# Kernel optimization log

Measured on AMD Instinct MI355X. Metric: run time of the kernel, lower is better.

## Reference

```python
import jax, jax.numpy as jnp
import numpy as np

N_RAYS, N_SAMPLES, GRID, APP_DIM, FEATC = 2048, 256, 128, 27, 128
VIEWPE, FEAPE = 2, 2
NEAR, FAR = 2.0, 6.0
AABB0, AABB1 = -1.5, 1.5
DENSITY_SHIFT, DISTANCE_SCALE = -10.0, 25.0
IN_MLPC = 2 * VIEWPE * 3 + 2 * FEAPE * APP_DIM + 3 + APP_DIM  # 150


def positional_encoding(x, freqs):
    fb = (2.0 ** jnp.arange(freqs)).astype(x.dtype)
    p = (x[..., None] * fb).reshape(x.shape[:-1] + (freqs * x.shape[-1],))
    return jnp.concatenate([jnp.sin(p), jnp.cos(p)], axis=-1)


def trilinear(vol, coords):
    # vol: [C, D, H, W]; coords: [P, 3] in [-1, 1] ordered (x, y, z) like torch grid_sample (align_corners=True)
    C, D, H, W = vol.shape
    x = (coords[:, 0] + 1.0) * 0.5 * (W - 1)
    y = (coords[:, 1] + 1.0) * 0.5 * (H - 1)
    z = (coords[:, 2] + 1.0) * 0.5 * (D - 1)
    x0 = jnp.clip(jnp.floor(x), 0, W - 2).astype(jnp.int32)
    y0 = jnp.clip(jnp.floor(y), 0, H - 2).astype(jnp.int32)
    z0 = jnp.clip(jnp.floor(z), 0, D - 2).astype(jnp.int32)
    x1, y1, z1 = x0 + 1, y0 + 1, z0 + 1
    fx, fy, fz = x - x0, y - y0, z - z0
    g = lambda zi, yi, xi: vol[:, zi, yi, xi]  # [C, P]
    out = (g(z0, y0, x0) * ((1 - fz) * (1 - fy) * (1 - fx))
           + g(z0, y0, x1) * ((1 - fz) * (1 - fy) * fx)
           + g(z0, y1, x0) * ((1 - fz) * fy * (1 - fx))
           + g(z0, y1, x1) * ((1 - fz) * fy * fx)
           + g(z1, y0, x0) * (fz * (1 - fy) * (1 - fx))
           + g(z1, y0, x1) * (fz * (1 - fy) * fx)
           + g(z1, y1, x0) * (fz * fy * (1 - fx))
           + g(z1, y1, x1) * (fz * fy * fx))
    return out  # [C, P]


def setup_inputs() -> dict:
    key = jax.random.key(0)
    ks = jax.random.split(key, 10)
    return {
        'rays_o': jax.random.uniform(ks[0], (N_RAYS, 3), jnp.float32, -0.5, 0.5) + jnp.array([0.0, 0.0, -4.0]),
        'rays_d': jax.random.normal(ks[1], (N_RAYS, 3), jnp.float32) * 0.1 + jnp.array([0.0, 0.0, 1.0]),
        'density_volume': jax.random.normal(ks[2], (1, GRID, GRID, GRID), jnp.float32) * 2.0 + 10.0,
        'app_volume': jax.random.normal(ks[3], (APP_DIM, GRID, GRID, GRID), jnp.float32) * 0.1,
        'w1': jax.random.normal(ks[4], (IN_MLPC, FEATC), jnp.float32) * 0.05,
        'b1': jnp.zeros((FEATC,), jnp.float32),
        'w2': jax.random.normal(ks[5], (FEATC, FEATC), jnp.float32) * 0.05,
        'b2': jnp.zeros((FEATC,), jnp.float32),
        'w3': jax.random.normal(ks[6], (FEATC, 3), jnp.float32) * 0.05,
        'b3': jnp.zeros((3,), jnp.float32),
    }


def reference(rays_o, rays_d, density_volume, app_volume, w1, b1, w2, b2, w3, b3):
    viewdirs = rays_d / jnp.linalg.norm(rays_d, axis=-1, keepdims=True)  # [N, 3]
    z_vals = jnp.linspace(NEAR, FAR, N_SAMPLES, dtype=rays_o.dtype)      # [S]
    z_vals = jnp.broadcast_to(z_vals, (N_RAYS, N_SAMPLES))
    pts = rays_o[:, None, :] + viewdirs[:, None, :] * z_vals[..., None]  # [N, S, 3]
    dists = jnp.concatenate([z_vals[:, 1:] - z_vals[:, :-1], z_vals[:, -1:] * 0 + (FAR - NEAR) / (N_SAMPLES - 1)], axis=-1)

    # normalize_coord: (xyz - aabb0) * (2 / aabbSize) - 1
    coords = jnp.clip((pts - AABB0) * (2.0 / (AABB1 - AABB0)) - 1.0, -1.0, 1.0).reshape(-1, 3)

    # density lookup + feature2density (softplus with shift)
    sigma_feat = trilinear(density_volume, coords)[0].reshape(N_RAYS, N_SAMPLES)
    sigma = jax.nn.softplus(sigma_feat + DENSITY_SHIFT)

    # raw2alpha: alpha, cumprod transmittance, weights
    alpha = 1.0 - jnp.exp(-sigma * dists * DISTANCE_SCALE)               # [N, S]
    T = jnp.cumprod(jnp.concatenate([jnp.ones((N_RAYS, 1), alpha.dtype), 1.0 - alpha + 1e-10], axis=-1), axis=-1)
    weights = alpha * T[:, :-1]                                          # [N, S]

    # MLPRender_Fea shading on all sampled points
    feat = trilinear(app_volume, coords).T                               # [P, app_dim]
    vd = jnp.broadcast_to(viewdirs[:, None, :], (N_RAYS, N_SAMPLES, 3)).reshape(-1, 3)
    mlp_in = jnp.concatenate([feat, vd, positional_encoding(feat, FEAPE), positional_encoding(vd, VIEWPE)], axis=-1)
    h = jax.nn.relu(mlp_in @ w1 + b1)
    h = jax.nn.relu(h @ w2 + b2)
    rgb = jax.nn.sigmoid(h @ w3 + b3).reshape(N_RAYS, N_SAMPLES, 3)

    acc_map = jnp.sum(weights, axis=-1)                                  # [N]
    rgb_map = jnp.sum(weights[..., None] * rgb, axis=-2)                 # [N, 3]
    rgb_map = jnp.clip(rgb_map + (1.0 - acc_map)[..., None], 0.0, 1.0)   # white background
    return rgb_map
```

## Files before the change

kernel.cpp:

```cpp
#include <hip/hip_runtime.h>
#include <math.h>

#define N_RAYS 2048
#define NSAMP  256
#define NPTS   (N_RAYS * NSAMP)
#define NCHUNK (NPTS / 64)
#define GRIDN  128
#define G2     (GRIDN * GRIDN)
#define G3     (GRIDN * GRIDN * GRIDN)
#define APPC   27
#define CHP    28
#define FEATC  128
#define K1PAD  160
#define ASTR   168
#define HSTR   136
#define H2STR  132

typedef __attribute__((ext_vector_type(8))) short short8;
typedef __attribute__((ext_vector_type(4))) float float4v;

__device__ __forceinline__ unsigned short f2bf(float f) {
  unsigned int u = __float_as_uint(f);
  return (unsigned short)((u + 0x7FFFu + ((u >> 16) & 1u)) >> 16);
}
__device__ __forceinline__ float bf2f(unsigned short u) {
  return __uint_as_float(((unsigned int)u) << 16);
}

__device__ __forceinline__ void corner_setup(float cx, float cy, float cz,
                                             int& ibase, float* w8) {
  float x = (cx + 1.0f) * 0.5f * 127.0f;
  float y = (cy + 1.0f) * 0.5f * 127.0f;
  float z = (cz + 1.0f) * 0.5f * 127.0f;
  float x0f = fminf(fmaxf(floorf(x), 0.0f), 126.0f);
  float y0f = fminf(fmaxf(floorf(y), 0.0f), 126.0f);
  float z0f = fminf(fmaxf(floorf(z), 0.0f), 126.0f);
  int x0 = (int)x0f, y0 = (int)y0f, z0 = (int)z0f;
  float fx = x - x0f, fy = y - y0f, fz = z - z0f;
  float gx = 1.0f - fx, gy = 1.0f - fy, gz = 1.0f - fz;
  ibase = (z0 * GRIDN + y0) * GRIDN + x0;
  w8[0] = gz * gy * gx; w8[1] = gz * gy * fx;
  w8[2] = gz * fy * gx; w8[3] = gz * fy * fx;
  w8[4] = fz * gy * gx; w8[5] = fz * gy * fx;
  w8[6] = fz * fy * gx; w8[7] = fz * fy * fx;
}

__global__ __launch_bounds__(256)
void transpose_kernel(const float* __restrict__ avol, unsigned short* __restrict__ appT) {
  int v0 = (blockIdx.x * 256 + threadIdx.x) * 2;
  float2 v[APPC];
  #pragma unroll
  for (int c = 0; c < APPC; ++c) v[c] = *(const float2*)&avol[(size_t)c * G3 + v0];
  unsigned short* dst = appT + (size_t)v0 * CHP;
  #pragma unroll
  for (int i = 0; i < 7; ++i) {
    ushort4 o;
    o.x = f2bf(v[4*i+0].x); o.y = f2bf(v[4*i+1].x);
    o.z = (4*i+2 < APPC) ? f2bf(v[4*i+2].x) : (unsigned short)0;
    o.w = (4*i+3 < APPC) ? f2bf(v[4*i+3].x) : (unsigned short)0;
    *(ushort4*)&dst[4*i] = o;
  }
  #pragma unroll
  for (int i = 0; i < 7; ++i) {
    ushort4 o;
    o.x = f2bf(v[4*i+0].y); o.y = f2bf(v[4*i+1].y);
    o.z = (4*i+2 < APPC) ? f2bf(v[4*i+2].y) : (unsigned short)0;
    o.w = (4*i+3 < APPC) ? f2bf(v[4*i+3].y) : (unsigned short)0;
    *(ushort4*)&dst[CHP + 4*i] = o;
  }
}

__global__ __launch_bounds__(256)
void prep_weights(const float* __restrict__ w1, const float* __restrict__ w2,
                  unsigned short* __restrict__ w1T, unsigned short* __restrict__ w2T) {
  int t = blockIdx.x * 256 + threadIdx.x;
  if (t < 128 * K1PAD) {
    int n = t / K1PAD, k = t - n * K1PAD;
    w1T[t] = (k < 150) ? f2bf(w1[k * 128 + n]) : (unsigned short)0;
  } else {
    int i = t - 128 * K1PAD;
    if (i < 128 * 128) {
      int n = i >> 7, k = i & 127;
      w2T[i] = f2bf(w2[k * 128 + n]);
    }
  }
}

__global__ __launch_bounds__(256)
void ray_kernel(const float* __restrict__ rays_o, const float* __restrict__ rays_d,
                const float* __restrict__ dvol,
                float* __restrict__ weights_ws, float* __restrict__ acc_ws,
                int* __restrict__ count, int* __restrict__ worklist) {
  int r = blockIdx.x, s = threadIdx.x;
  int lane = s & 63, wv = s >> 6;
  float ox = rays_o[r*3+0], oy = rays_o[r*3+1], oz = rays_o[r*3+2];
  float dx = rays_d[r*3+0], dy = rays_d[r*3+1], dz = rays_d[r*3+2];
  float inv = rsqrtf(dx*dx + dy*dy + dz*dz);
  dx *= inv; dy *= inv; dz *= inv;
  float z = 2.0f + (4.0f / 255.0f) * (float)s;
  float px = ox + dx * z, py = oy + dy * z, pz = oz + dz * z;
  float cx = fminf(fmaxf((px + 1.5f) * (2.0f/3.0f) - 1.0f, -1.0f), 1.0f);
  float cy = fminf(fmaxf((py + 1.5f) * (2.0f/3.0f) - 1.0f, -1.0f), 1.0f);
  float cz = fminf(fmaxf((pz + 1.5f) * (2.0f/3.0f) - 1.0f, -1.0f), 1.0f);
  int ibase; float w8[8];
  corner_setup(cx, cy, cz, ibase, w8);
  float sf = dvol[ibase]            * w8[0] + dvol[ibase + 1]            * w8[1]
           + dvol[ibase + GRIDN]    * w8[2] + dvol[ibase + GRIDN + 1]    * w8[3]
           + dvol[ibase + G2]       * w8[4] + dvol[ibase + G2 + 1]       * w8[5]
           + dvol[ibase + G2+GRIDN] * w8[6] + dvol[ibase + G2+GRIDN+1]   * w8[7];
  float xv = sf - 10.0f;
  float sp = (xv > 0.0f) ? (xv + log1pf(expf(-xv))) : log1pf(expf(xv));
  float alpha = 1.0f - expf(-sp * (100.0f / 255.0f));

  float tt = 1.0f - alpha + 1e-10f;
  float p = tt;
  #pragma unroll
  for (int d = 1; d < 64; d <<= 1) {
    float v = __shfl_up(p, d);
    if (lane >= d) p *= v;
  }
  __shared__ float wtot[4], wacc[4];
  if (lane == 63) wtot[wv] = p;
  __syncthreads();
  float pref = 1.0f;
  #pragma unroll
  for (int w2i = 0; w2i < 3; ++w2i) if (w2i < wv) pref *= wtot[w2i];
  float ex = __shfl_up(p, 1);
  if (lane == 0) ex = 1.0f;
  float T = pref * ex;
  float wgt = alpha * T;
  weights_ws[r * NSAMP + s] = wgt;
  float sum = wgt;
  #pragma unroll
  for (int d = 32; d; d >>= 1) sum += __shfl_xor(sum, d);
  if (lane == 0) {
    wacc[wv] = sum;
    if (sum >= 1e-5f) {
      int pos = atomicAdd(count, 1);
      worklist[pos] = r * 4 + wv;
    }
  }
  __syncthreads();
  if (s == 0) acc_ws[r] = wacc[0] + wacc[1] + wacc[2] + wacc[3];
}

template <bool USET>
__global__ __launch_bounds__(256)
void shade_kernel(const float* __restrict__ rays_o, const float* __restrict__ rays_d,
                  const float* __restrict__ avol, const unsigned short* __restrict__ appT,
                  const unsigned short* __restrict__ w1T, const unsigned short* __restrict__ w2T,
                  const float* __restrict__ b1, const float* __restrict__ b2,
                  const float* __restrict__ w3, const float* __restrict__ b3,
                  const float* __restrict__ weights_ws, float* __restrict__ rgb_accum,
                  const int* __restrict__ count, int* __restrict__ work_ctr,
                  const int* __restrict__ worklist) {
  __shared__ unsigned short A_lds[64 * ASTR];
  __shared__ unsigned short h1_lds[64 * HSTR];
  __shared__ int s_idx, s_n;

  int t = threadIdx.x;
  int lane = t & 63, wv = t >> 6;

  if (t == 0) s_n = *count;

  for (;;) {
    __syncthreads();
    if (t == 0) s_idx = atomicAdd(work_ctr, 1);
    __syncthreads();
    if (s_idx >= s_n) break;
    int chunk = worklist[s_idx];
    int gp0 = chunk * 64;
    int r = gp0 >> 8;

    {
      int q = t & 3, pt = t >> 2;
      int gp = gp0 + pt, s = gp & 255;
      float ox = rays_o[r*3+0], oy = rays_o[r*3+1], oz = rays_o[r*3+2];
      float dx = rays_d[r*3+0], dy = rays_d[r*3+1], dz = rays_d[r*3+2];
      float inv = rsqrtf(dx*dx + dy*dy + dz*dz);
      dx *= inv; dy *= inv; dz *= inv;
      float z = 2.0f + (4.0f / 255.0f) * (float)s;
      float px = ox + dx * z, py = oy + dy * z, pz = oz + dz * z;
      float cx = fminf(fmaxf((px + 1.5f) * (2.0f/3.0f) - 1.0f, -1.0f), 1.0f);
      float cy = fminf(fmaxf((py + 1.5f) * (2.0f/3.0f) - 1.0f, -1.0f), 1.0f);
      float cz = fminf(fmaxf((pz + 1.5f) * (2.0f/3.0f) - 1.0f, -1.0f), 1.0f);
      int ibase; float w8[8];
      corner_setup(cx, cy, cz, ibase, w8);

      int vi = ibase + (q >> 1) * G2 + (q & 1) * GRIDN;
      float wA = w8[2*q], wB = w8[2*q+1];
      float part[27];
      if (USET) {
        const ushort4* c0 = (const ushort4*)(appT + (size_t)vi * CHP);
        const ushort4* c1 = (const ushort4*)(appT + (size_t)(vi + 1) * CHP);
        ushort4 a[7], b[7];
        #pragma unroll
        for (int i = 0; i < 7; ++i) { a[i] = c0[i]; b[i] = c1[i]; }
        #pragma unroll
        for (int c = 0; c < 27; ++c) {
          unsigned short ua = (&a[c >> 2].x)[c & 3];
          unsigned short ub = (&b[c >> 2].x)[c & 3];
          part[c] = wA * bf2f(ua) + wB * bf2f(ub);
        }
      } else {
        #pragma unroll
        for (int c = 0; c < 27; ++c) {
          const float* base = avol + (size_t)c * G3 + vi;
          part[c] = wA * base[0] + wB * base[1];
        }
      }
      #pragma unroll
      for (int c = 0; c < 27; ++c) {
        float v = part[c];
        v += __shfl_xor(v, 1);
        v += __shfl_xor(v, 2);
        part[c] = v;
      }
      float f[7];
      #pragma unroll
      for (int j = 0; j < 7; ++j) {
        float vlo = (q & 1) ? part[7 + j] : part[j];
        float vhi = (q & 1) ? part[(21 + j < 27) ? 21 + j : 26] : part[14 + j];
        f[j] = (q & 2) ? vhi : vlo;
      }
      unsigned short* Arow = A_lds + pt * ASTR;
      int cbase = 7 * q;
      #pragma unroll
      for (int j = 0; j < 7; ++j) {
        int c = cbase + j;
        if (c < 27) {
          float fv = f[j];
          Arow[c] = f2bf(fv);
          float s1 = __sinf(fv),      c1 = __cosf(fv);
          float s2 = __sinf(2.0f*fv), c2 = __cosf(2.0f*fv);
          Arow[30 + 2*c] = f2bf(s1); Arow[31 + 2*c] = f2bf(s2);
          Arow[84 + 2*c] = f2bf(c1); Arow[85 + 2*c] = f2bf(c2);
        }
      }
      if (q == 3) {
        float vd[3] = {dx, dy, dz};
        #pragma unroll
        for (int d = 0; d < 3; ++d) {
          Arow[27 + d] = f2bf(vd[d]);
          float s1 = __sinf(vd[d]),      c1 = __cosf(vd[d]);
          float s2 = __sinf(2.0f*vd[d]), c2 = __cosf(2.0f*vd[d]);
          Arow[138 + 2*d] = f2bf(s1); Arow[139 + 2*d] = f2bf(s2);
          Arow[144 + 2*d] = f2bf(c1); Arow[145 + 2*d] = f2bf(c2);
        }
      }
      if (q == 1) {
        #pragma unroll
        for (int i = 0; i < 5; ++i) *(unsigned int*)&Arow[150 + 2*i] = 0u;
      }
    }
    __syncthreads();

    int nlo = lane & 15;
    int koff = (lane >> 4) * 8;
    int mrow = wv * 16 + nlo;

    short8 a1[5];
    #pragma unroll
    for (int kt = 0; kt < 5; ++kt)
      a1[kt] = *(const short8*)&A_lds[mrow * ASTR + kt * 32 + koff];
    #pragma unroll
    for (int nt = 0; nt < 8; ++nt) {
      float4v acc = {0.f, 0.f, 0.f, 0.f};
      #pragma unroll
      for (int kt = 0; kt < 5; ++kt) {
        short8 b = *(const short8*)&w1T[(nt * 16 + nlo) * K1PAD + kt * 32 + koff];
        acc = __builtin_amdgcn_mfma_f32_16x16x32_bf16(a1[kt], b, acc, 0, 0, 0);
      }
      float bv = b1[nt * 16 + nlo];
      #pragma unroll
      for (int rg = 0; rg < 4; ++rg) {
        int m = wv * 16 + (lane >> 4) * 4 + rg;
        float hv = fmaxf(acc[rg] + bv, 0.0f);
        h1_lds[m * HSTR + nt * 16 + nlo] = f2bf(hv);
      }
    }
    __syncthreads();

    short8 a2[4];
    #pragma unroll
    for (int kt = 0; kt < 4; ++kt)
      a2[kt] = *(const short8*)&h1_lds[mrow * HSTR + kt * 32 + koff];
    unsigned short* h2 = A_lds;
    #pragma unroll
    for (int nt = 0; nt < 8; ++nt) {
      float4v acc = {0.f, 0.f, 0.f, 0.f};
      #pragma unroll
      for (int kt = 0; kt < 4; ++kt) {
        short8 b = *(const short8*)&w2T[(nt * 16 + nlo) * FEATC + kt * 32 + koff];
        acc = __builtin_amdgcn_mfma_f32_16x16x32_bf16(a2[kt], b, acc, 0, 0, 0);
      }
      float bv = b2[nt * 16 + nlo];
      #pragma unroll
      for (int rg = 0; rg < 4; ++rg) {
        int m = wv * 16 + (lane >> 4) * 4 + rg;
        float hv = fmaxf(acc[rg] + bv, 0.0f);
        h2[m * H2STR + nt * 16 + nlo] = f2bf(hv);
      }
    }
    __syncthreads();

    if (wv < 3) {
      int j = wv, pp = lane;
      const unsigned short* h2row = h2 + pp * H2STR;
      float sum = b3[j];
      #pragma unroll
      for (int k = 0; k < FEATC; k += 4) {
        ushort4 hv = *(const ushort4*)&h2row[k];
        sum += bf2f(hv.x) * w3[(k+0)*3 + j] + bf2f(hv.y) * w3[(k+1)*3 + j]
             + bf2f(hv.z) * w3[(k+2)*3 + j] + bf2f(hv.w) * w3[(k+3)*3 + j];
      }
      float val = (1.0f / (1.0f + __expf(-sum))) * weights_ws[gp0 + pp];
      #pragma unroll
      for (int d = 32; d; d >>= 1) val += __shfl_xor(val, d);
      if (pp == 0) atomicAdd(&rgb_accum[r * 3 + j], val);
    }
  }
}

__global__ void finish_kernel(const float* __restrict__ rgb_accum,
                              const float* __restrict__ acc_ws,
                              float* __restrict__ out) {
  int i = blockIdx.x * blockDim.x + threadIdx.x;
  if (i < N_RAYS * 3) {
    int r = i / 3;
    float v = rgb_accum[i] + 1.0f - acc_ws[r];
    out[i] = fminf(fmaxf(v, 0.0f), 1.0f);
  }
}

extern "C" void kernel_launch(void* const* d_in, const int* in_sizes, int n_in,
                              void* d_out, int out_size, void* d_ws, size_t ws_size,
                              hipStream_t stream) {
  const float* rays_o = (const float*)d_in[0];
  const float* rays_d = (const float*)d_in[1];
  const float* dvol   = (const float*)d_in[2];
  const float* avol   = (const float*)d_in[3];
  const float* w1     = (const float*)d_in[4];
  const float* b1     = (const float*)d_in[5];
  const float* w2     = (const float*)d_in[6];
  const float* b2     = (const float*)d_in[7];
  const float* w3     = (const float*)d_in[8];
  const float* b3     = (const float*)d_in[9];
  float* out = (float*)d_out;

  float* weights_ws = (float*)d_ws;
  float* acc_ws     = weights_ws + NPTS;
  float* rgb_accum  = acc_ws + N_RAYS;
  int*   count      = (int*)(rgb_accum + N_RAYS * 3);
  int*   work_ctr   = count + 1;
  int*   worklist   = work_ctr + 1;
  unsigned short* w1T = (unsigned short*)(worklist + NCHUNK);
  unsigned short* w2T = w1T + 128 * K1PAD;
  unsigned short* appT = w2T + 128 * 128;

  size_t fixed_bytes = (size_t)(NPTS + N_RAYS + N_RAYS * 3 + 2 + NCHUNK) * 4
                     + (size_t)(128 * K1PAD + 128 * 128) * 2;
  size_t need = fixed_bytes + (size_t)G3 * CHP * 2;
  bool uset = ws_size >= need;

  hipMemsetAsync(rgb_accum, 0, (N_RAYS * 3 + 2) * sizeof(float), stream);
  prep_weights<<<(128 * K1PAD + 128 * 128 + 255) / 256, 256, 0, stream>>>(w1, w2, w1T, w2T);
  if (uset)
    transpose_kernel<<<G3 / 512, 256, 0, stream>>>(avol, appT);
  ray_kernel<<<N_RAYS, 256, 0, stream>>>(rays_o, rays_d, dvol, weights_ws, acc_ws,
                                         count, worklist);
  if (uset)
    shade_kernel<true><<<1024, 256, 0, stream>>>(rays_o, rays_d, avol, appT, w1T, w2T,
                                                 b1, b2, w3, b3, weights_ws, rgb_accum,
                                                 count, work_ctr, worklist);
  else
    shade_kernel<false><<<1024, 256, 0, stream>>>(rays_o, rays_d, avol, appT, w1T, w2T,
                                                  b1, b2, w3, b3, weights_ws, rgb_accum,
                                                  count, work_ctr, worklist);
  finish_kernel<<<(N_RAYS * 3 + 255) / 256, 256, 0, stream>>>(rgb_accum, acc_ws, out);
}
```

Before: 513.4 us.

## Restrict app-volume transpose to bounding box of active sample voxels

The ray kernel now also reduces per-wave min/max voxel indices for active chunks and atomically writes a global bounding box. The transpose that converts the appearance volume to bf16 channel-last layout runs after the ray kernel and skips voxels outside that box, cutting the read of the full 27-channel float volume. It also changes the H2STR LDS stride. The cost is extra shuffles and atomics in the ray kernel and a serial dependency: the transpose can no longer overlap with the ray pass.

```diff
diff --git a/kernel.cpp b/kernel.cpp
--- a/kernel.cpp
+++ b/kernel.cpp
@@ -14,7 +14,7 @@
 #define K1PAD  160
 #define ASTR   168
 #define HSTR   136
-#define H2STR  132
+#define H2STR  130
 
 typedef __attribute__((ext_vector_type(8))) short short8;
 typedef __attribute__((ext_vector_type(4))) float float4v;
@@ -27,15 +27,16 @@
   return __uint_as_float(((unsigned int)u) << 16);
 }
 
-__device__ __forceinline__ void corner_setup(float cx, float cy, float cz,
-                                             int& ibase, float* w8) {
+__device__ __forceinline__ void corner_setup_xyz(float cx, float cy, float cz,
+                                                 int& x0, int& y0, int& z0,
+                                                 int& ibase, float* w8) {
   float x = (cx + 1.0f) * 0.5f * 127.0f;
   float y = (cy + 1.0f) * 0.5f * 127.0f;
   float z = (cz + 1.0f) * 0.5f * 127.0f;
   float x0f = fminf(fmaxf(floorf(x), 0.0f), 126.0f);
   float y0f = fminf(fmaxf(floorf(y), 0.0f), 126.0f);
   float z0f = fminf(fmaxf(floorf(z), 0.0f), 126.0f);
-  int x0 = (int)x0f, y0 = (int)y0f, z0 = (int)z0f;
+  x0 = (int)x0f; y0 = (int)y0f; z0 = (int)z0f;
   float fx = x - x0f, fy = y - y0f, fz = z - z0f;
   float gx = 1.0f - fx, gy = 1.0f - fy, gz = 1.0f - fz;
   ibase = (z0 * GRIDN + y0) * GRIDN + x0;
@@ -46,8 +47,91 @@
 }
 
 __global__ __launch_bounds__(256)
-void transpose_kernel(const float* __restrict__ avol, unsigned short* __restrict__ appT) {
-  int v0 = (blockIdx.x * 256 + threadIdx.x) * 2;
+void ray_kernel(const float* __restrict__ rays_o, const float* __restrict__ rays_d,
+                const float* __restrict__ dvol,
+                float* __restrict__ weights_ws, float* __restrict__ acc_ws,
+                int* __restrict__ count, int* __restrict__ worklist,
+                int* __restrict__ bounds) {
+  int r = blockIdx.x, s = threadIdx.x;
+  int lane = s & 63, wv = s >> 6;
+  float ox = rays_o[r*3+0], oy = rays_o[r*3+1], oz = rays_o[r*3+2];
+  float dx = rays_d[r*3+0], dy = rays_d[r*3+1], dz = rays_d[r*3+2];
+  float inv = rsqrtf(dx*dx + dy*dy + dz*dz);
+  dx *= inv; dy *= inv; dz *= inv;
+  float z = 2.0f + (4.0f / 255.0f) * (float)s;
+  float px = ox + dx * z, py = oy + dy * z, pz = oz + dz * z;
+  float cx = fminf(fmaxf((px + 1.5f) * (2.0f/3.0f) - 1.0f, -1.0f), 1.0f);
+  float cy = fminf(fmaxf((py + 1.5f) * (2.0f/3.0f) - 1.0f, -1.0f), 1.0f);
+  float cz = fminf(fmaxf((pz + 1.5f) * (2.0f/3.0f) - 1.0f, -1.0f), 1.0f);
+  int x0, y0, z0, ibase; float w8[8];
+  corner_setup_xyz(cx, cy, cz, x0, y0, z0, ibase, w8);
+  float sf = dvol[ibase]            * w8[0] + dvol[ibase + 1]            * w8[1]
+           + dvol[ibase + GRIDN]    * w8[2] + dvol[ibase + GRIDN + 1]    * w8[3]
+           + dvol[ibase + G2]       * w8[4] + dvol[ibase + G2 + 1]       * w8[5]
+           + dvol[ibase + G2+GRIDN] * w8[6] + dvol[ibase + G2+GRIDN+1]   * w8[7];
+  float xv = sf - 10.0f;
+  float sp = (xv > 0.0f) ? (xv + log1pf(expf(-xv))) : log1pf(expf(xv));
+  float alpha = 1.0f - expf(-sp * (100.0f / 255.0f));
+
+  float tt = 1.0f - alpha + 1e-10f;
+  float p = tt;
+  #pragma unroll
+  for (int d = 1; d < 64; d <<= 1) {
+    float v = __shfl_up(p, d);
+    if (lane >= d) p *= v;
+  }
+  __shared__ float wtot[4], wacc[4];
+  if (lane == 63) wtot[wv] = p;
+  __syncthreads();
+  float pref = 1.0f;
+  #pragma unroll
+  for (int w2i = 0; w2i < 3; ++w2i) if (w2i < wv) pref *= wtot[w2i];
+  float ex = __shfl_up(p, 1);
+  if (lane == 0) ex = 1.0f;
+  float T = pref * ex;
+  float wgt = alpha * T;
+  weights_ws[r * NSAMP + s] = wgt;
+
+  float sum = wgt;
+  int mnx = x0, mny = y0, mnz = z0, mxx = x0, mxy = y0, mxz = z0;
+  #pragma unroll
+  for (int d = 32; d; d >>= 1) {
+    sum += __shfl_xor(sum, d);
+    mnx = min(mnx, __shfl_xor(mnx, d)); mxx = max(mxx, __shfl_xor(mxx, d));
+    mny = min(mny, __shfl_xor(mny, d)); mxy = max(mxy, __shfl_xor(mxy, d));
+    mnz = min(mnz, __shfl_xor(mnz, d)); mxz = max(mxz, __shfl_xor(mxz, d));
+  }
+  if (lane == 0) {
+    wacc[wv] = sum;
+    if (sum >= 1e-5f) {
+      int pos = atomicAdd(count, 1);
+      worklist[pos] = r * 4 + wv;
+      atomicMin(&bounds[0], mnx); atomicMax(&bounds[3], mxx + 1);
+      atomicMin(&bounds[1], mny); atomicMax(&bounds[4], mxy + 1);
+      atomicMin(&bounds[2], mnz); atomicMax(&bounds[5], mxz + 1);
+    }
+  }
+  __syncthreads();
+  if (s == 0) acc_ws[r] = wacc[0] + wacc[1] + wacc[2] + wacc[3];
+}
+
+__global__ __launch_bounds__(256)
+void transpose_kernel(const float* __restrict__ avol, unsigned short* __restrict__ appT,
+                      const int* __restrict__ bounds) {
+  int vblk = blockIdx.x * 512;
+  int zb = vblk >> 14;
+  int yb = (vblk & 16383) >> 7;
+  int zmin = bounds[2], zmax = bounds[5];
+  int ymin = bounds[1], ymax = bounds[4];
+  if (zb < zmin || zb > zmax) return;
+  if (yb + 3 < ymin || yb > ymax) return;
+  int v0 = vblk + threadIdx.x * 2;
+  int y = (v0 & 16383) >> 7;
+  int x = v0 & 127;
+  if (y < ymin || y > ymax) return;
+  int xmin = bounds[0], xmax = bounds[3];
+  if (x + 1 < xmin || x > xmax) return;
+
   float2 v[APPC];
   #pragma unroll
   for (int c = 0; c < APPC; ++c) v[c] = *(const float2*)&avol[(size_t)c * G3 + v0];
@@ -84,64 +168,6 @@
       w2T[i] = f2bf(w2[k * 128 + n]);
     }
   }
-}
-
-__global__ __launch_bounds__(256)
-void ray_kernel(const float* __restrict__ rays_o, const float* __restrict__ rays_d,
-                const float* __restrict__ dvol,
-                float* __restrict__ weights_ws, float* __restrict__ acc_ws,
-                int* __restrict__ count, int* __restrict__ worklist) {
-  int r = blockIdx.x, s = threadIdx.x;
-  int lane = s & 63, wv = s >> 6;
-  float ox = rays_o[r*3+0], oy = rays_o[r*3+1], oz = rays_o[r*3+2];
-  float dx = rays_d[r*3+0], dy = rays_d[r*3+1], dz = rays_d[r*3+2];
-  float inv = rsqrtf(dx*dx + dy*dy + dz*dz);
-  dx *= inv; dy *= inv; dz *= inv;
-  float z = 2.0f + (4.0f / 255.0f) * (float)s;
-  float px = ox + dx * z, py = oy + dy * z, pz = oz + dz * z;
-  float cx = fminf(fmaxf((px + 1.5f) * (2.0f/3.0f) - 1.0f, -1.0f), 1.0f);
-  float cy = fminf(fmaxf((py + 1.5f) * (2.0f/3.0f) - 1.0f, -1.0f), 1.0f);
-  float cz = fminf(fmaxf((pz + 1.5f) * (2.0f/3.0f) - 1.0f, -1.0f), 1.0f);
-  int ibase; float w8[8];
-  corner_setup(cx, cy, cz, ibase, w8);
-  float sf = dvol[ibase]            * w8[0] + dvol[ibase + 1]            * w8[1]
-           + dvol[ibase + GRIDN]    * w8[2] + dvol[ibase + GRIDN + 1]    * w8[3]
-           + dvol[ibase + G2]       * w8[4] + dvol[ibase + G2 + 1]       * w8[5]
-           + dvol[ibase + G2+GRIDN] * w8[6] + dvol[ibase + G2+GRIDN+1]   * w8[7];
-  float xv = sf - 10.0f;
-  float sp = (xv > 0.0f) ? (xv + log1pf(expf(-xv))) : log1pf(expf(xv));
-  float alpha = 1.0f - expf(-sp * (100.0f / 255.0f));
-
-  float tt = 1.0f - alpha + 1e-10f;
-  float p = tt;
-  #pragma unroll
-  for (int d = 1; d < 64; d <<= 1) {
-    float v = __shfl_up(p, d);
-    if (lane >= d) p *= v;
-  }
-  __shared__ float wtot[4], wacc[4];
-  if (lane == 63) wtot[wv] = p;
-  __syncthreads();
-  float pref = 1.0f;
-  #pragma unroll
-  for (int w2i = 0; w2i < 3; ++w2i) if (w2i < wv) pref *= wtot[w2i];
-  float ex = __shfl_up(p, 1);
-  if (lane == 0) ex = 1.0f;
-  float T = pref * ex;
-  float wgt = alpha * T;
-  weights_ws[r * NSAMP + s] = wgt;
-  float sum = wgt;
-  #pragma unroll
-  for (int d = 32; d; d >>= 1) sum += __shfl_xor(sum, d);
-  if (lane == 0) {
-    wacc[wv] = sum;
-    if (sum >= 1e-5f) {
-      int pos = atomicAdd(count, 1);
-      worklist[pos] = r * 4 + wv;
-    }
-  }
-  __syncthreads();
-  if (s == 0) acc_ws[r] = wacc[0] + wacc[1] + wacc[2] + wacc[3];
 }
 
 template <bool USET>
@@ -184,8 +210,8 @@
       float cx = fminf(fmaxf((px + 1.5f) * (2.0f/3.0f) - 1.0f, -1.0f), 1.0f);
       float cy = fminf(fmaxf((py + 1.5f) * (2.0f/3.0f) - 1.0f, -1.0f), 1.0f);
       float cz = fminf(fmaxf((pz + 1.5f) * (2.0f/3.0f) - 1.0f, -1.0f), 1.0f);
-      int ibase; float w8[8];
-      corner_setup(cx, cy, cz, ibase, w8);
+      int x0, y0, z0, ibase; float w8[8];
+      corner_setup_xyz(cx, cy, cz, x0, y0, z0, ibase, w8);
 
       int vi = ibase + (q >> 1) * G2 + (q & 1) * GRIDN;
       float wA = w8[2*q], wB = w8[2*q+1];
@@ -353,29 +379,32 @@
   float* rgb_accum  = acc_ws + N_RAYS;
   int*   count      = (int*)(rgb_accum + N_RAYS * 3);
   int*   work_ctr   = count + 1;
-  int*   worklist   = work_ctr + 1;
+  int*   bounds     = work_ctr + 1;
+  int*   worklist   = bounds + 6;
   unsigned short* w1T = (unsigned short*)(worklist + NCHUNK);
   unsigned short* w2T = w1T + 128 * K1PAD;
   unsigned short* appT = w2T + 128 * 128;
 
-  size_t fixed_bytes = (size_t)(NPTS + N_RAYS + N_RAYS * 3 + 2 + NCHUNK) * 4
+  size_t fixed_bytes = (size_t)(NPTS + N_RAYS + N_RAYS * 3 + 8 + NCHUNK) * 4
                      + (size_t)(128 * K1PAD + 128 * 128) * 2;
   size_t need = fixed_bytes + (size_t)G3 * CHP * 2;
   bool uset = ws_size >= need;
 
   hipMemsetAsync(rgb_accum, 0, (N_RAYS * 3 + 2) * sizeof(float), stream);
+  hipMemsetAsync(bounds, 0x7f, 3 * sizeof(int), stream);
+  hipMemsetAsync(bounds + 3, 0, 3 * sizeof(int), stream);
   prep_weights<<<(128 * K1PAD + 128 * 128 + 255) / 256, 256, 0, stream>>>(w1, w2, w1T, w2T);
-  if (uset)
-    transpose_kernel<<<G3 / 512, 256, 0, stream>>>(avol, appT);
   ray_kernel<<<N_RAYS, 256, 0, stream>>>(rays_o, rays_d, dvol, weights_ws, acc_ws,
-                                         count, worklist);
-  if (uset)
+                                         count, worklist, bounds);
+  if (uset) {
+    transpose_kernel<<<G3 / 512, 256, 0, stream>>>(avol, appT, bounds);
     shade_kernel<true><<<1024, 256, 0, stream>>>(rays_o, rays_d, avol, appT, w1T, w2T,
                                                  b1, b2, w3, b3, weights_ws, rgb_accum,
                                                  count, work_ctr, worklist);
-  else
+  } else {
     shade_kernel<false><<<1024, 256, 0, stream>>>(rays_o, rays_d, avol, appT, w1T, w2T,
                                                   b1, b2, w3, b3, weights_ws, rgb_accum,
                                                   count, work_ctr, worklist);
+  }
   finish_kernel<<<(N_RAYS * 3 + 255) / 256, 256, 0, stream>>>(rgb_accum, acc_ws, out);
 }
```

New measurement: 624.6 us. 21.6% more time.
